# Performance work log

Measured on AMD Instinct MI355X. Metric: run time of the kernel, lower is better.

## Reference

```python
import jax, jax.numpy as jnp
import numpy as np

B, S, D = 2, 2048, 1024
H = 16
HD = D // H  # 64


def _rope_tables(seq_len, head_dim, dtype=jnp.float32):
    inv_freq = 1.0 / (10000.0 ** (jnp.arange(0, head_dim, 2, dtype=jnp.float32) / head_dim))
    t = jnp.arange(seq_len, dtype=jnp.float32)
    freqs = jnp.einsum('i,j->ij', t, inv_freq)            # [S, HD/2]
    emb = jnp.concatenate([freqs, freqs], axis=-1)        # [S, HD]
    return jnp.cos(emb).astype(dtype)[None, None], jnp.sin(emb).astype(dtype)[None, None]


def _rotate_half(x):
    x1, x2 = x[..., : x.shape[-1] // 2], x[..., x.shape[-1] // 2 :]
    return jnp.concatenate([-x2, x1], axis=-1)


def setup_inputs() -> dict:
    key = jax.random.key(0)
    ks = jax.random.split(key, 9)
    s = 0.02
    return {
        'hidden_states': jax.random.normal(ks[0], (B, S, D), jnp.float32),
        'attention_mask': jnp.zeros((B, 1, S, S), jnp.float32),
        'Wq': jax.random.normal(ks[1], (D, D), jnp.float32) * s,
        'bq': jnp.zeros((D,), jnp.float32),
        'Wk': jax.random.normal(ks[2], (D, D), jnp.float32) * s,
        'bk': jnp.zeros((D,), jnp.float32),
        'Wv': jax.random.normal(ks[3], (D, D), jnp.float32) * s,
        'bv': jnp.zeros((D,), jnp.float32),
        'Wo': jax.random.normal(ks[4], (D, D), jnp.float32) * s,
        'bo': jnp.zeros((D,), jnp.float32),
    }


def reference(hidden_states, attention_mask, Wq, bq, Wk, bk, Wv, bv, Wo, bo):
    b, s = hidden_states.shape[:2]
    q = hidden_states @ Wq.T + bq
    k = hidden_states @ Wk.T + bk
    v = hidden_states @ Wv.T + bv
    # [B, H, S, HD]
    q = q.reshape(b, s, H, HD).transpose(0, 2, 1, 3)
    k = k.reshape(b, s, H, HD).transpose(0, 2, 1, 3)
    v = v.reshape(b, s, H, HD).transpose(0, 2, 1, 3)
    cos, sin = _rope_tables(s, HD, q.dtype)
    q = q * cos + _rotate_half(q) * sin
    k = k * cos + _rotate_half(k) * sin
    scaling = HD ** (-0.5)
    scores = jnp.einsum('bhqd,bhkd->bhqk', q, k) * scaling
    scores = scores / jnp.log(jnp.asarray(float(s), scores.dtype))  # dynamic NTK
    scores = scores + attention_mask
    probs = jax.nn.softmax(scores, axis=-1)
    out = jnp.einsum('bhqk,bhkd->bhqd', probs, v)
    out = out.transpose(0, 2, 1, 3).reshape(b, s, H * HD)
    return out @ Wo.T + bo
```

## Files before the change

kernel.cpp:

```cpp
#include <hip/hip_runtime.h>
#include <math.h>

#define S_LEN 2048
#define NHEAD 16
#define HDIM  64

typedef __attribute__((ext_vector_type(8))) short bf16x8;
typedef __attribute__((ext_vector_type(4))) float f32x4;

__device__ __forceinline__ unsigned short f2bf(float f) {
    union { float f; unsigned u; } v; v.f = f;
    unsigned r = v.u + 0x7fffu + ((v.u >> 16) & 1u);
    return (unsigned short)(r >> 16);
}

__device__ __forceinline__ void gl2lds16(const void* g, void* l) {
    __builtin_amdgcn_global_load_lds(
        (__attribute__((address_space(1))) void*)(void*)(g),
        (__attribute__((address_space(3))) void*)(l), 16, 0, 0);
}

__global__ __launch_bounds__(256) void rope_tab_kernel(float2* __restrict__ tab)
{
    const int gid = blockIdx.x * 256 + threadIdx.x;
    const int s = gid >> 5, i = gid & 31;
    const float l2c = 0.41524101186092029f;
    const float freq = exp2f(-(float)i * l2c);
    const float ang = (float)s * freq;
    float2 cs;
    cs.x = cosf(ang);
    cs.y = sinf(ang);
    tab[gid] = cs;
}

__global__ __launch_bounds__(256) void convert_kernel(
    const float* __restrict__ hs, const float* __restrict__ Wq,
    const float* __restrict__ Wk, const float* __restrict__ Wv,
    const float* __restrict__ Wo, unsigned short* __restrict__ dst)
{
    const int gid = blockIdx.x * 256 + threadIdx.x;
    const int n = gid << 2;
    const float* src; int off;
    if (n < (4 << 20))      { src = hs; off = n; }
    else if (n < (5 << 20)) { src = Wq; off = n - (4 << 20); }
    else if (n < (6 << 20)) { src = Wk; off = n - (5 << 20); }
    else if (n < (7 << 20)) { src = Wv; off = n - (6 << 20); }
    else                    { src = Wo; off = n - (7 << 20); }
    const float4 v = *(const float4*)(src + off);
    ushort4 o;
    o.x = f2bf(v.x); o.y = f2bf(v.y); o.z = f2bf(v.z); o.w = f2bf(v.w);
    *(ushort4*)(dst + n) = o;
}

__global__ __launch_bounds__(256, 3) void qkv_gemm_kernel(
    const unsigned short* __restrict__ X,
    const unsigned short* __restrict__ Wall,
    const float* __restrict__ bq, const float* __restrict__ bk,
    const float* __restrict__ bv, const float2* __restrict__ rtab,
    unsigned short* __restrict__ qo, unsigned short* __restrict__ ko,
    unsigned short* __restrict__ vo)
{
    __shared__ unsigned short As[128 * 64];
    __shared__ unsigned short Bs[128 * 64];

    const int mat = blockIdx.x >> 3;
    const int n0  = (blockIdx.x & 7) << 7;
    const int m0  = blockIdx.y << 7;
    const unsigned short* W = Wall + (mat << 20);
    const float* bias = (mat == 0) ? bq : (mat == 1) ? bk : bv;
    unsigned short* out = (mat == 0) ? qo : (mat == 1) ? ko : vo;

    const int tid = threadIdx.x;
    const int wave = tid >> 6, lane = tid & 63;
    const int quad = lane >> 4, ln = lane & 15;
    const int wm = (wave >> 1) << 6, wn = (wave & 1) << 6;

    f32x4 acc[4][4] = {};

    for (int k0 = 0; k0 < 1024; k0 += 64) {
        #pragma unroll
        for (int L = 0; L < 4; ++L) {
            const int i = tid + (L << 8);
            const int r = i >> 3, cl = i & 7;
            const int cg = (cl ^ (r & 7)) << 3;
            gl2lds16(X + (m0 + r) * 1024 + k0 + cg, &As[i << 3]);
            gl2lds16(W + (n0 + r) * 1024 + k0 + cg, &Bs[i << 3]);
        }
        __syncthreads();
        #pragma unroll
        for (int s = 0; s < 2; ++s) {
            bf16x8 a[4], b[4];
            #pragma unroll
            for (int t = 0; t < 4; ++t) {
                const int ra = wm + (t << 4) + ln;
                a[t] = *(const bf16x8*)&As[(ra << 6) + ((((s << 2) | quad) ^ (ra & 7)) << 3)];
                const int rb = wn + (t << 4) + ln;
                b[t] = *(const bf16x8*)&Bs[(rb << 6) + ((((s << 2) | quad) ^ (rb & 7)) << 3)];
            }
            #pragma unroll
            for (int i = 0; i < 4; ++i)
                #pragma unroll
                for (int j = 0; j < 4; ++j)
                    acc[i][j] = __builtin_amdgcn_mfma_f32_16x16x32_bf16(a[i], b[j], acc[i][j], 0, 0, 0);
        }
        __syncthreads();
    }

    float bv4[4];
    #pragma unroll
    for (int jt = 0; jt < 4; ++jt) bv4[jt] = bias[n0 + wn + (jt << 4) + ln];

    const int h = (n0 + wn) >> 6;

    #pragma unroll
    for (int i = 0; i < 4; ++i) {
        #pragma unroll
        for (int reg = 0; reg < 4; ++reg) {
            const int m = m0 + wm + (i << 4) + (quad << 2) + reg;
            const int b_ = m >> 11, s_ = m & 2047;
            unsigned short* o = out + ((((b_ << 4) + h) << 11) + s_) * 64;
            if (mat < 2) {
                #pragma unroll
                for (int jl = 0; jl < 2; ++jl) {
                    const int hd = (jl << 4) + ln;
                    const float2 cs = rtab[(s_ << 5) + hd];
                    const float x1 = acc[i][jl][reg] + bv4[jl];
                    const float x2 = acc[i][jl + 2][reg] + bv4[jl + 2];
                    o[hd]      = f2bf(x1 * cs.x - x2 * cs.y);
                    o[hd + 32] = f2bf(x2 * cs.x + x1 * cs.y);
                }
            } else {
                #pragma unroll
                for (int jt = 0; jt < 4; ++jt) {
                    const int hd = (jt << 4) + ln;
                    o[hd] = f2bf(acc[i][jt][reg] + bv4[jt]);
                }
            }
        }
    }
}

__global__ __launch_bounds__(256) void vtrans_kernel(
    const unsigned short* __restrict__ v, unsigned short* __restrict__ vt)
{
    __shared__ unsigned short T[64][66];
    const int bh = blockIdx.x >> 5;
    const int s0 = (blockIdx.x & 31) << 6;
    const int tid = threadIdx.x;
    #pragma unroll
    for (int L = 0; L < 4; ++L) {
        const int i = tid + (L << 8);
        const int r = i >> 4, c4 = (i & 15) << 2;
        const ushort4 in = *(const ushort4*)(v + ((bh << 11) + s0 + r) * 64 + c4);
        T[r][c4 + 0] = in.x; T[r][c4 + 1] = in.y;
        T[r][c4 + 2] = in.z; T[r][c4 + 3] = in.w;
    }
    __syncthreads();
    #pragma unroll
    for (int L = 0; L < 4; ++L) {
        const int i = tid + (L << 8);
        const int hd = i >> 4, b = i & 15;
        ushort4 o;
        o.x = T[b][hd];      o.y = T[b + 16][hd];
        o.z = T[b + 32][hd]; o.w = T[b + 48][hd];
        *(ushort4*)(vt + ((bh << 6) + hd) * 2048 + s0 + (b << 2)) = o;
    }
}

__global__ __launch_bounds__(256, 4) void flash_kernel(
    const unsigned short* __restrict__ qb, const unsigned short* __restrict__ kb,
    const unsigned short* __restrict__ vtb, const float* __restrict__ mask,
    unsigned short* __restrict__ attn)
{
    __shared__ unsigned short Ks[2][64 * 64];
    __shared__ unsigned short Vt[2][64 * 64];
    __shared__ unsigned short Ps[64 * 64];

    const int qt = blockIdx.x & 31;
    const int bh = blockIdx.x >> 5;
    const int b_ = bh >> 4, h = bh & 15;
    const int q0 = qt << 6;

    const int tid = threadIdx.x;
    const int wave = tid >> 6, lane = tid & 63;
    const int quad = lane >> 4, ln = lane & 15;

    const unsigned short* qrow = qb + ((size_t)((bh << 11) + q0 + (wave << 4) + ln) << 6);
    bf16x8 qa[2];
    qa[0] = *(const bf16x8*)(qrow + (quad << 3));
    qa[1] = *(const bf16x8*)(qrow + 32 + (quad << 3));

    const float scale = 0.125f / logf(2048.0f);

    const float* mbase = mask + ((size_t)b_ << 22)
                       + ((size_t)(q0 + (wave << 4) + (quad << 2)) << 11) + ln;

    unsigned short* Pw = Ps + (wave << 10);

    float l_i[4] = {0.f, 0.f, 0.f, 0.f};
    f32x4 O[4] = {};

    #pragma unroll
    for (int L = 0; L < 2; ++L) {
        const int i = tid + (L << 8);
        const int r = i >> 3, cl = i & 7;
        const int cg = (cl ^ (r & 7)) << 3;
        gl2lds16(kb + ((bh << 11) + r) * 64 + cg, &Ks[0][i << 3]);
        gl2lds16(vtb + ((bh << 6) + r) * 2048 + cg, &Vt[0][i << 3]);
    }
    float mcur[4][4];
    #pragma unroll
    for (int reg = 0; reg < 4; ++reg)
        #pragma unroll
        for (int j = 0; j < 4; ++j)
            mcur[reg][j] = mbase[(reg << 11) + (j << 4)];

    for (int kt = 0; kt < 32; ++kt) {
        const int cur = kt & 1;

        __syncthreads();

        float mnext[4][4];
        if (kt < 31) {
            const int kn = (kt + 1) << 6;
            #pragma unroll
            for (int L = 0; L < 2; ++L) {
                const int i = tid + (L << 8);
                const int r = i >> 3, cl = i & 7;
                const int cg = (cl ^ (r & 7)) << 3;
                gl2lds16(kb + ((bh << 11) + kn + r) * 64 + cg, &Ks[cur ^ 1][i << 3]);
                gl2lds16(vtb + ((bh << 6) + r) * 2048 + kn + cg, &Vt[cur ^ 1][i << 3]);
            }
            #pragma unroll
            for (int reg = 0; reg < 4; ++reg)
                #pragma unroll
                for (int j = 0; j < 4; ++j)
                    mnext[reg][j] = mbase[(reg << 11) + kn + (j << 4)];
        }

        f32x4 sacc[4] = {};
        #pragma unroll
        for (int s = 0; s < 2; ++s) {
            bf16x8 bfr[4];
            #pragma unroll
            for (int j = 0; j < 4; ++j) {
                const int r = (j << 4) + ln;
                bfr[j] = *(const bf16x8*)&Ks[cur][(r << 6) + ((((s << 2) | quad) ^ (r & 7)) << 3)];
            }
            #pragma unroll
            for (int j = 0; j < 4; ++j)
                sacc[j] = __builtin_amdgcn_mfma_f32_16x16x32_bf16(qa[s], bfr[j], sacc[j], 0, 0, 0);
        }

        #pragma unroll
        for (int reg = 0; reg < 4; ++reg) {
            const int pr = (quad << 2) + reg;
            float p[4];
            #pragma unroll
            for (int j = 0; j < 4; ++j) {
                p[j] = __expf(fmaf(sacc[j][reg], scale, mcur[reg][j]));
                l_i[reg] += p[j];
            }
            unsigned u0 = __float_as_uint(p[0]) + 0x8000u;
            unsigned u1 = __float_as_uint(p[1]) + 0x8000u;
            unsigned u2 = __float_as_uint(p[2]) + 0x8000u;
            unsigned u3 = __float_as_uint(p[3]) + 0x8000u;
            uint2 w;
            w.x = __builtin_amdgcn_perm(u1, u0, 0x07060302u);
            w.y = __builtin_amdgcn_perm(u3, u2, 0x07060302u);
            const int e = (pr << 6) + ((((ln >> 1) ^ (pr & 7)) << 3)) + ((ln & 1) << 2);
            *(uint2*)&Pw[e] = w;
        }

        #pragma unroll
        for (int s = 0; s < 2; ++s) {
            const bf16x8 a = *(const bf16x8*)&Pw[(ln << 6) + ((((s << 2) | quad) ^ (ln & 7)) << 3)];
            bf16x8 bfr[4];
            #pragma unroll
            for (int j = 0; j < 4; ++j) {
                const int r = (j << 4) + ln;
                bfr[j] = *(const bf16x8*)&Vt[cur][(r << 6) + ((((s << 2) | quad) ^ (r & 7)) << 3)];
            }
            #pragma unroll
            for (int j = 0; j < 4; ++j)
                O[j] = __builtin_amdgcn_mfma_f32_16x16x32_bf16(a, bfr[j], O[j], 0, 0, 0);
        }

        if (kt < 31) {
            #pragma unroll
            for (int reg = 0; reg < 4; ++reg)
                #pragma unroll
                for (int j = 0; j < 4; ++j)
                    mcur[reg][j] = mnext[reg][j];
        }
    }

    #pragma unroll
    for (int reg = 0; reg < 4; ++reg) {
        float l = l_i[reg];
        l += __shfl_xor(l, 1);
        l += __shfl_xor(l, 2);
        l += __shfl_xor(l, 4);
        l += __shfl_xor(l, 8);
        const float inv = 1.0f / l;
        const int qr = q0 + (wave << 4) + (quad << 2) + reg;
        unsigned short* op = attn + (((size_t)((b_ << 11) + qr)) << 10) + (h << 6);
        #pragma unroll
        for (int j = 0; j < 4; ++j)
            op[(j << 4) + ln] = f2bf(O[j][reg] * inv);
    }
}

__global__ __launch_bounds__(256, 3) void out_gemm_kernel(
    const unsigned short* __restrict__ X, const unsigned short* __restrict__ W,
    const float* __restrict__ bias, float* __restrict__ out)
{
    __shared__ unsigned short As[128 * 64];
    __shared__ unsigned short Bs[128 * 64];

    const int n0 = blockIdx.x << 7;
    const int m0 = blockIdx.y << 7;
    const int tid = threadIdx.x;
    const int wave = tid >> 6, lane = tid & 63;
    const int quad = lane >> 4, ln = lane & 15;
    const int wm = (wave >> 1) << 6, wn = (wave & 1) << 6;

    f32x4 acc[4][4] = {};

    for (int k0 = 0; k0 < 1024; k0 += 64) {
        #pragma unroll
        for (int L = 0; L < 4; ++L) {
            const int i = tid + (L << 8);
            const int r = i >> 3, cl = i & 7;
            const int cg = (cl ^ (r & 7)) << 3;
            gl2lds16(X + (m0 + r) * 1024 + k0 + cg, &As[i << 3]);
            gl2lds16(W + (n0 + r) * 1024 + k0 + cg, &Bs[i << 3]);
        }
        __syncthreads();
        #pragma unroll
        for (int s = 0; s < 2; ++s) {
            bf16x8 a[4], b[4];
            #pragma unroll
            for (int t = 0; t < 4; ++t) {
                const int ra = wm + (t << 4) + ln;
                a[t] = *(const bf16x8*)&As[(ra << 6) + ((((s << 2) | quad) ^ (ra & 7)) << 3)];
                const int rb = wn + (t << 4) + ln;
                b[t] = *(const bf16x8*)&Bs[(rb << 6) + ((((s << 2) | quad) ^ (rb & 7)) << 3)];
            }
            #pragma unroll
            for (int i = 0; i < 4; ++i)
                #pragma unroll
                for (int j = 0; j < 4; ++j)
                    acc[i][j] = __builtin_amdgcn_mfma_f32_16x16x32_bf16(a[i], b[j], acc[i][j], 0, 0, 0);
        }
        __syncthreads();
    }

    float bv4[4];
    #pragma unroll
    for (int jt = 0; jt < 4; ++jt) bv4[jt] = bias[n0 + wn + (jt << 4) + ln];

    #pragma unroll
    for (int i = 0; i < 4; ++i)
        #pragma unroll
        for (int reg = 0; reg < 4; ++reg) {
            const int m = m0 + wm + (i << 4) + (quad << 2) + reg;
            #pragma unroll
            for (int jt = 0; jt < 4; ++jt) {
                const int n = n0 + wn + (jt << 4) + ln;
                out[m * 1024 + n] = acc[i][jt][reg] + bv4[jt];
            }
        }
}

extern "C" void kernel_launch(void* const* d_in, const int* in_sizes, int n_in,
                              void* d_out, int out_size, void* d_ws, size_t ws_size,
                              hipStream_t stream)
{
    const float* hs   = (const float*)d_in[0];
    const float* mask = (const float*)d_in[1];
    const float* Wq   = (const float*)d_in[2];
    const float* bq   = (const float*)d_in[3];
    const float* Wk   = (const float*)d_in[4];
    const float* bk   = (const float*)d_in[5];
    const float* Wv   = (const float*)d_in[6];
    const float* bv   = (const float*)d_in[7];
    const float* Wo   = (const float*)d_in[8];
    const float* bo   = (const float*)d_in[9];

    unsigned short* ws = (unsigned short*)d_ws;
    const size_t M1 = (size_t)1 << 20;
    unsigned short* hsb   = ws;
    unsigned short* wall  = ws + 4 * M1;
    unsigned short* wob   = ws + 7 * M1;
    unsigned short* qbf   = ws + 8 * M1;
    unsigned short* kbf   = ws + 12 * M1;
    unsigned short* vbf   = ws + 16 * M1;
    unsigned short* vtb   = ws + 20 * M1;
    unsigned short* attnb = ws + 24 * M1;
    float2*         rtab  = (float2*)(ws + 28 * M1);

    rope_tab_kernel<<<256, 256, 0, stream>>>(rtab);
    convert_kernel<<<8192, 256, 0, stream>>>(hs, Wq, Wk, Wv, Wo, ws);
    qkv_gemm_kernel<<<dim3(24, 32), 256, 0, stream>>>(hsb, wall, bq, bk, bv, rtab, qbf, kbf, vbf);
    vtrans_kernel<<<1024, 256, 0, stream>>>(vbf, vtb);
    flash_kernel<<<1024, 256, 0, stream>>>(qbf, kbf, vtb, mask, attnb);
    out_gemm_kernel<<<dim3(8, 32), 256, 0, stream>>>(attnb, wob, bo, (float*)d_out);
}
```

Baseline: 242.7 us.

## Vectorize attention mask loads via permuted K rows and fuse rope table into convert

Permutes the key row order loaded into shared memory so each lane's four score columns map to four contiguous mask entries, allowing float4 mask loads instead of scalar strided loads. The V transpose kernel is changed to natural order to match the new key ordering. The RoPE table computation is folded into the convert kernel as extra blocks, removing a launch. The risk is index consistency between the P and V orderings.

```diff
diff --git a/kernel.cpp b/kernel.cpp
--- a/kernel.cpp
+++ b/kernel.cpp
@@ -20,25 +20,26 @@
         (__attribute__((address_space(3))) void*)(l), 16, 0, 0);
 }
 
-__global__ __launch_bounds__(256) void rope_tab_kernel(float2* __restrict__ tab)
-{
-    const int gid = blockIdx.x * 256 + threadIdx.x;
-    const int s = gid >> 5, i = gid & 31;
-    const float l2c = 0.41524101186092029f;
-    const float freq = exp2f(-(float)i * l2c);
-    const float ang = (float)s * freq;
-    float2 cs;
-    cs.x = cosf(ang);
-    cs.y = sinf(ang);
-    tab[gid] = cs;
-}
-
 __global__ __launch_bounds__(256) void convert_kernel(
     const float* __restrict__ hs, const float* __restrict__ Wq,
     const float* __restrict__ Wk, const float* __restrict__ Wv,
-    const float* __restrict__ Wo, unsigned short* __restrict__ dst)
-{
-    const int gid = blockIdx.x * 256 + threadIdx.x;
+    const float* __restrict__ Wo, unsigned short* __restrict__ dst,
+    float2* __restrict__ rtab)
+{
+    const int bid = blockIdx.x;
+    if (bid >= 8192) {
+        const int gid = (bid - 8192) * 256 + threadIdx.x;
+        const int s = gid >> 5, i = gid & 31;
+        const float l2c = 0.41524101186092029f;
+        const float freq = exp2f(-(float)i * l2c);
+        const float ang = (float)s * freq;
+        float2 cs;
+        cs.x = cosf(ang);
+        cs.y = sinf(ang);
+        rtab[gid] = cs;
+        return;
+    }
+    const int gid = bid * 256 + threadIdx.x;
     const int n = gid << 2;
     const float* src; int off;
     if (n < (4 << 20))      { src = hs; off = n; }
@@ -159,11 +160,11 @@
     #pragma unroll
     for (int L = 0; L < 4; ++L) {
         const int i = tid + (L << 8);
-        const int hd = i >> 4, b = i & 15;
+        const int hd = i >> 4, c4 = (i & 15) << 2;
         ushort4 o;
-        o.x = T[b][hd];      o.y = T[b + 16][hd];
-        o.z = T[b + 32][hd]; o.w = T[b + 48][hd];
-        *(ushort4*)(vt + ((bh << 6) + hd) * 2048 + s0 + (b << 2)) = o;
+        o.x = T[c4 + 0][hd]; o.y = T[c4 + 1][hd];
+        o.z = T[c4 + 2][hd]; o.w = T[c4 + 3][hd];
+        *(ushort4*)(vt + ((bh << 6) + hd) * 2048 + s0 + c4) = o;
     }
 }
 
@@ -193,49 +194,47 @@
     const float scale = 0.125f / logf(2048.0f);
 
     const float* mbase = mask + ((size_t)b_ << 22)
-                       + ((size_t)(q0 + (wave << 4) + (quad << 2)) << 11) + ln;
+                       + ((size_t)(q0 + (wave << 4) + (quad << 2)) << 11) + (ln << 2);
 
     unsigned short* Pw = Ps + (wave << 10);
+
+    const int i0 = tid, i1 = tid + 256;
+    const int r0 = i0 >> 3, c0 = ((i0 & 7) ^ (r0 & 7)) << 3;
+    const int r1 = i1 >> 3, c1 = ((i1 & 7) ^ (r1 & 7)) << 3;
+    const int p0 = ((r0 & 15) << 2) + (r0 >> 4);
+    const int p1 = ((r1 & 15) << 2) + (r1 >> 4);
+    const unsigned short* kg0 = kb + ((bh << 11) + p0) * 64 + c0;
+    const unsigned short* kg1 = kb + ((bh << 11) + p1) * 64 + c1;
+    const unsigned short* vg0 = vtb + ((bh << 6) + r0) * 2048 + c0;
+    const unsigned short* vg1 = vtb + ((bh << 6) + r1) * 2048 + c1;
 
     float l_i[4] = {0.f, 0.f, 0.f, 0.f};
     f32x4 O[4] = {};
 
-    #pragma unroll
-    for (int L = 0; L < 2; ++L) {
-        const int i = tid + (L << 8);
-        const int r = i >> 3, cl = i & 7;
-        const int cg = (cl ^ (r & 7)) << 3;
-        gl2lds16(kb + ((bh << 11) + r) * 64 + cg, &Ks[0][i << 3]);
-        gl2lds16(vtb + ((bh << 6) + r) * 2048 + cg, &Vt[0][i << 3]);
-    }
-    float mcur[4][4];
+    gl2lds16(kg0, &Ks[0][i0 << 3]);
+    gl2lds16(kg1, &Ks[0][i1 << 3]);
+    gl2lds16(vg0, &Vt[0][i0 << 3]);
+    gl2lds16(vg1, &Vt[0][i1 << 3]);
+    float4 mcur[4];
     #pragma unroll
     for (int reg = 0; reg < 4; ++reg)
-        #pragma unroll
-        for (int j = 0; j < 4; ++j)
-            mcur[reg][j] = mbase[(reg << 11) + (j << 4)];
+        mcur[reg] = *(const float4*)(mbase + (reg << 11));
 
     for (int kt = 0; kt < 32; ++kt) {
         const int cur = kt & 1;
 
         __syncthreads();
 
-        float mnext[4][4];
+        float4 mnext[4];
         if (kt < 31) {
             const int kn = (kt + 1) << 6;
-            #pragma unroll
-            for (int L = 0; L < 2; ++L) {
-                const int i = tid + (L << 8);
-                const int r = i >> 3, cl = i & 7;
-                const int cg = (cl ^ (r & 7)) << 3;
-                gl2lds16(kb + ((bh << 11) + kn + r) * 64 + cg, &Ks[cur ^ 1][i << 3]);
-                gl2lds16(vtb + ((bh << 6) + r) * 2048 + kn + cg, &Vt[cur ^ 1][i << 3]);
-            }
+            gl2lds16(kg0 + (kn << 6), &Ks[cur ^ 1][i0 << 3]);
+            gl2lds16(kg1 + (kn << 6), &Ks[cur ^ 1][i1 << 3]);
+            gl2lds16(vg0 + kn, &Vt[cur ^ 1][i0 << 3]);
+            gl2lds16(vg1 + kn, &Vt[cur ^ 1][i1 << 3]);
             #pragma unroll
             for (int reg = 0; reg < 4; ++reg)
-                #pragma unroll
-                for (int j = 0; j < 4; ++j)
-                    mnext[reg][j] = mbase[(reg << 11) + kn + (j << 4)];
+                mnext[reg] = *(const float4*)(mbase + kn + (reg << 11));
         }
 
         f32x4 sacc[4] = {};
@@ -255,12 +254,14 @@
         #pragma unroll
         for (int reg = 0; reg < 4; ++reg) {
             const int pr = (quad << 2) + reg;
+            const float m0f = mcur[reg].x, m1f = mcur[reg].y,
+                        m2f = mcur[reg].z, m3f = mcur[reg].w;
             float p[4];
-            #pragma unroll
-            for (int j = 0; j < 4; ++j) {
-                p[j] = __expf(fmaf(sacc[j][reg], scale, mcur[reg][j]));
-                l_i[reg] += p[j];
-            }
+            p[0] = __expf(fmaf(sacc[0][reg], scale, m0f));
+            p[1] = __expf(fmaf(sacc[1][reg], scale, m1f));
+            p[2] = __expf(fmaf(sacc[2][reg], scale, m2f));
+            p[3] = __expf(fmaf(sacc[3][reg], scale, m3f));
+            l_i[reg] += (p[0] + p[1]) + (p[2] + p[3]);
             unsigned u0 = __float_as_uint(p[0]) + 0x8000u;
             unsigned u1 = __float_as_uint(p[1]) + 0x8000u;
             unsigned u2 = __float_as_uint(p[2]) + 0x8000u;
@@ -289,9 +290,7 @@
         if (kt < 31) {
             #pragma unroll
             for (int reg = 0; reg < 4; ++reg)
-                #pragma unroll
-                for (int j = 0; j < 4; ++j)
-                    mcur[reg][j] = mnext[reg][j];
+                mcur[reg] = mnext[reg];
         }
     }
 
@@ -400,8 +399,7 @@
     unsigned short* attnb = ws + 24 * M1;
     float2*         rtab  = (float2*)(ws + 28 * M1);
 
-    rope_tab_kernel<<<256, 256, 0, stream>>>(rtab);
-    convert_kernel<<<8192, 256, 0, stream>>>(hs, Wq, Wk, Wv, Wo, ws);
+    convert_kernel<<<8448, 256, 0, stream>>>(hs, Wq, Wk, Wv, Wo, ws, rtab);
     qkv_gemm_kernel<<<dim3(24, 32), 256, 0, stream>>>(hsb, wall, bq, bk, bv, rtab, qbf, kbf, vbf);
     vtrans_kernel<<<1024, 256, 0, stream>>>(vbf, vtb);
     flash_kernel<<<1024, 256, 0, stream>>>(qbf, kbf, vtb, mask, attnb);
```

Result: faster. 237.9 us (-2.0%).
